# Optimization experiments

Measured on AMD Instinct MI355X. Metric: run time of the kernel, lower is better.

The kernel has to match this reference:

```python
import jax, jax.numpy as jnp
import numpy as np

NUM_CAMS, NUM_LEVELS, NUM_PTS, NUM_GROUPS = 6, 4, 13, 8


def grid_sample(fm, grid):
    """Bilinear grid_sample, align_corners=False, zeros padding.
    fm: (N,C,H,W); grid: (N,P,Q,2) xy in [-1,1] -> (N,C,P,Q)."""
    N, C, H, W = fm.shape
    x, y = grid[..., 0], grid[..., 1]
    ix = ((x + 1.0) * W - 1.0) * 0.5
    iy = ((y + 1.0) * H - 1.0) * 0.5
    ix0f = jnp.floor(ix)
    iy0f = jnp.floor(iy)
    wx1 = ix - ix0f
    wy1 = iy - iy0f
    wx0 = 1.0 - wx1
    wy0 = 1.0 - wy1
    ix0 = ix0f.astype(jnp.int32)
    iy0 = iy0f.astype(jnp.int32)
    flat = fm.reshape(N, C, H * W)

    def gather(iyc, ixc):
        valid = ((ixc >= 0) & (ixc < W) & (iyc >= 0) & (iyc < H)).astype(fm.dtype)
        idx = jnp.clip(iyc, 0, H - 1) * W + jnp.clip(ixc, 0, W - 1)
        g = jnp.take_along_axis(flat, idx.reshape(N, 1, -1), axis=2)
        return g.reshape((N, C) + idx.shape[1:]) * valid[:, None]

    v00 = gather(iy0, ix0)
    v01 = gather(iy0, ix0 + 1)
    v10 = gather(iy0 + 1, ix0)
    v11 = gather(iy0 + 1, ix0 + 1)
    return (v00 * (wy0 * wx0)[:, None] + v01 * (wy0 * wx1)[:, None]
            + v10 * (wy1 * wx0)[:, None] + v11 * (wy1 * wx1)[:, None])


def setup_inputs() -> dict:
    key = jax.random.key(0)
    ks = jax.random.split(key, 16)
    bs, NA, E = 2, 900, 256
    shapes = [(12, E, 64, 176), (12, E, 32, 88), (12, E, 16, 44), (12, E, 8, 22)]
    proj = jnp.eye(4, dtype=jnp.float32)[None, None] + 0.1 * jax.random.normal(ks[0], (bs, NUM_CAMS, 4, 4), jnp.float32)
    return {
        "instance_feature": jax.random.normal(ks[1], (bs, NA, E), jnp.float32),
        "anchor": jax.random.normal(ks[2], (bs, NA, E), jnp.float32),
        "anchor_embed": jax.random.normal(ks[3], (bs, NA, E), jnp.float32),
        "fm0": jax.random.normal(ks[4], shapes[0], jnp.float32),
        "fm1": jax.random.normal(ks[5], shapes[1], jnp.float32),
        "fm2": jax.random.normal(ks[6], shapes[2], jnp.float32),
        "fm3": jax.random.normal(ks[7], shapes[3], jnp.float32),
        "projection_mat": proj,
        "W_kps": 0.02 * jax.random.normal(ks[8], (E, NUM_PTS * 3), jnp.float32),
        "b_kps": jnp.zeros((NUM_PTS * 3,), jnp.float32),
        "W_wfc": 0.02 * jax.random.normal(ks[9], (E, NUM_GROUPS * NUM_CAMS * NUM_LEVELS * NUM_PTS), jnp.float32),
        "b_wfc": jnp.zeros((NUM_GROUPS * NUM_CAMS * NUM_LEVELS * NUM_PTS,), jnp.float32),
        "W_out": 0.02 * jax.random.normal(ks[10], (E, E), jnp.float32),
        "b_out": jnp.zeros((E,), jnp.float32),
    }


def reference(instance_feature, anchor, anchor_embed, fm0, fm1, fm2, fm3,
              projection_mat, W_kps, b_kps, W_wfc, b_wfc, W_out, b_out):
    bs, NA, E = instance_feature.shape
    C, L, P, G = NUM_CAMS, NUM_LEVELS, NUM_PTS, NUM_GROUPS
    gd = E // G
    # key points: anchor center + learned offsets (kps_generator)
    offs = (instance_feature @ W_kps + b_kps).reshape(bs, NA, P, 3)
    key_points = anchor[:, :, None, :3] + offs  # (bs,NA,P,3)
    # fusion weights: softmax over cam*level*pt slots, per group
    feat = instance_feature + anchor_embed
    w = (feat @ W_wfc + b_wfc).reshape(bs, NA, C * L * P, G)
    w = jax.nn.softmax(w, axis=-2)
    # project points to 2D
    pts = jnp.concatenate([key_points, jnp.ones_like(key_points[..., :1])], axis=-1)
    p2d = jnp.einsum('bcij,bnpj->bcnpi', projection_mat, pts)  # (bs,C,NA,P,4)
    depth = 1.0 / jnp.clip(p2d[..., 2:3], 1e-5)
    grid = (p2d[..., :2] * depth).reshape(bs * C, NA, P, 2)
    # multi-level bilinear sampling
    samples = [grid_sample(fm, grid) for fm in (fm0, fm1, fm2, fm3)]  # (bs*C,E,NA,P)
    feats = jnp.concatenate(samples, axis=3)  # (bs*C,E,NA,L*P)
    feats = feats.reshape(bs, C, E, NA, L * P).transpose(0, 3, 1, 4, 2)
    feats = feats.reshape(bs, NA, C * L * P, E)
    # grouped weighted fusion over all cam/level/pt slots
    fused = (w[..., None] * feats.reshape(bs, NA, C * L * P, G, gd)).sum(axis=2)
    fused = fused.reshape(bs, NA, E)
    out = fused @ W_out + b_out
    return out + instance_feature
```

## Files before the change

kernel.cpp:

```cpp
#include <hip/hip_runtime.h>
#include <hip/hip_bf16.h>

#define C_NUM_CAMS 6
#define C_NUM_LEVELS 4
#define C_NUM_PTS 13
#define C_NUM_GROUPS 8
#define C_BS 2
#define C_NA 900
#define C_E 256
#define C_NSLOT 312
#define C_NCOL 2496
#define C_NANCH 1800

#define LB0 0
#define LB1 34603008
#define LB2 43253760
#define LB3 45416448
#define FM8_WS_BYTES 45957120ull
#define WGT_WS_BYTES 17971200ull
#define WBT_WS_BYTES 1277952ull

typedef float floatx2 __attribute__((ext_vector_type(2)));
typedef float f32x4 __attribute__((ext_vector_type(4)));
typedef short s16x8 __attribute__((ext_vector_type(8)));
typedef float f32x4v __attribute__((ext_vector_type(4)));

static __device__ __forceinline__ int pk_fp8(float a, float b, float c, float d) {
  int v = __builtin_amdgcn_cvt_pk_fp8_f32(a, b, 0, false);
  v = __builtin_amdgcn_cvt_pk_fp8_f32(c, d, v, true);
  return v;
}
static __device__ __forceinline__ unsigned short f2bf(float f) {
  __hip_bfloat16 h = __float2bfloat16(f);
  return *reinterpret_cast<unsigned short*>(&h);
}

__global__ __launch_bounds__(256) void dfa_prep_wbt(
    const float* __restrict__ W, unsigned short* __restrict__ Wbt) {
  __shared__ unsigned short tile[64][264];
  int t = threadIdx.x;
  int c0 = blockIdx.x * 64;
  int rA = t >> 4;
  int cA = (t & 15) * 4;
#pragma unroll
  for (int p = 0; p < 16; ++p) {
    int r = p * 16 + rA;
    f32x4 v = *(const f32x4*)(W + (size_t)r * C_NCOL + c0 + cA);
    tile[cA + 0][r] = f2bf(v.x);
    tile[cA + 1][r] = f2bf(v.y);
    tile[cA + 2][r] = f2bf(v.z);
    tile[cA + 3][r] = f2bf(v.w);
  }
  __syncthreads();
  int cB = t >> 5;
  int i4 = t & 31;
#pragma unroll
  for (int p = 0; p < 8; ++p) {
    int c = p * 8 + cB;
    int4 o = *(const int4*)&tile[c][i4 * 8];
    *(int4*)(Wbt + (size_t)(c0 + c) * 256 + i4 * 8) = o;
  }
}

__global__ __launch_bounds__(256) void dfa_stage1(
    const float* __restrict__ fm0, const float* __restrict__ fm1,
    const float* __restrict__ fm2, const float* __restrict__ fm3,
    unsigned char* __restrict__ outw,
    const float* __restrict__ IF, const float* __restrict__ AE,
    const unsigned short* __restrict__ Wbt, const float* __restrict__ bwfc,
    float* __restrict__ logits) {
  __shared__ __align__(16) char smem[66560];
  int id = blockIdx.x;
  int t = threadIdx.x;
  int w = t >> 6, lane = t & 63;

  if (id >= 300) {
    int tid = id - 300;
    int (*lds)[260] = (int(*)[260])smem;
    const float* fm;
    int HW, strips;
    long long base;
    int rem;
    if (tid < 528)      { rem = tid;       fm = fm0; HW = 11264; strips = 44; base = LB0; }
    else if (tid < 660) { rem = tid - 528; fm = fm1; HW = 2816;  strips = 11; base = LB1; }
    else if (tid < 696) { rem = tid - 660; fm = fm2; HW = 704;   strips = 3;  base = LB2; }
    else                { rem = tid - 696; fm = fm3; HW = 176;   strips = 1;  base = LB3; }
    int img = rem / strips;
    int px0 = (rem % strips) * 256;

    {
      int pxl = lane * 4;
      bool pv = (px0 + pxl) < HW;
      const float* src = fm + (size_t)img * 256 * HW + px0 + pxl;
      if (pv) {
#pragma unroll 4
        for (int cq = 0; cq < 16; ++cq) {
          int ch = w * 64 + cq * 4;
          const float* s = src + (size_t)ch * HW;
          f32x4 r0 = *(const f32x4*)(s);
          f32x4 r1 = *(const f32x4*)(s + HW);
          f32x4 r2 = *(const f32x4*)(s + 2 * (size_t)HW);
          f32x4 r3 = *(const f32x4*)(s + 3 * (size_t)HW);
          int4 o;
          o.x = pk_fp8(r0.x, r1.x, r2.x, r3.x);
          o.y = pk_fp8(r0.y, r1.y, r2.y, r3.y);
          o.z = pk_fp8(r0.z, r1.z, r2.z, r3.z);
          o.w = pk_fp8(r0.w, r1.w, r2.w, r3.w);
          *(int4*)&lds[w * 16 + cq][pxl] = o;
        }
      }
    }
    __syncthreads();
    {
      int cq16 = (lane & 15) * 4;
      int pxs = lane >> 4;
#pragma unroll 4
      for (int i = 0; i < 16; ++i) {
        int px = w * 64 + i * 4 + pxs;
        if (px0 + px < HW) {
          int4 o;
          o.x = lds[cq16 + 0][px];
          o.y = lds[cq16 + 1][px];
          o.z = lds[cq16 + 2][px];
          o.w = lds[cq16 + 3][px];
          *(int4*)(outw + base + ((long long)img * HW + px0 + px) * 256 + cq16 * 4) = o;
        }
      }
    }
  } else {
    typedef unsigned short us40[40];
    us40* As = (us40*)smem;
    us40* Bs = (us40*)(smem + 10240);
    int rem = id;
    int m0 = (rem % 15) * 128;
    int n0 = (rem / 15) * 128;

    f32x4v acc[4][4];
#pragma unroll
    for (int mi = 0; mi < 4; ++mi)
#pragma unroll
      for (int ni = 0; ni < 4; ++ni)
        acc[mi][ni] = (f32x4v){0.f, 0.f, 0.f, 0.f};

    int r = t >> 1;
    int half = (t & 1) * 16;
    int wr = (w >> 1) * 64, wc = (w & 1) * 64;
    int rsel = lane & 15;
    int koff = (lane >> 4) * 8;

    for (int ks = 0; ks < 8; ++ks) {
      int k0 = ks * 32;
      {
        int a = m0 + r;
        s16x8 o0 = {0, 0, 0, 0, 0, 0, 0, 0};
        s16x8 o1 = {0, 0, 0, 0, 0, 0, 0, 0};
        if (a < C_NANCH) {
          const float* pI = IF + (size_t)a * 256 + k0 + half;
          const float* pA = AE + (size_t)a * 256 + k0 + half;
          f32x4 i0 = *(const f32x4*)(pI + 0), i1 = *(const f32x4*)(pI + 4);
          f32x4 i2 = *(const f32x4*)(pI + 8), i3 = *(const f32x4*)(pI + 12);
          f32x4 a0 = *(const f32x4*)(pA + 0), a1 = *(const f32x4*)(pA + 4);
          f32x4 a2 = *(const f32x4*)(pA + 8), a3 = *(const f32x4*)(pA + 12);
          o0[0] = (short)f2bf(i0.x + a0.x); o0[1] = (short)f2bf(i0.y + a0.y);
          o0[2] = (short)f2bf(i0.z + a0.z); o0[3] = (short)f2bf(i0.w + a0.w);
          o0[4] = (short)f2bf(i1.x + a1.x); o0[5] = (short)f2bf(i1.y + a1.y);
          o0[6] = (short)f2bf(i1.z + a1.z); o0[7] = (short)f2bf(i1.w + a1.w);
          o1[0] = (short)f2bf(i2.x + a2.x); o1[1] = (short)f2bf(i2.y + a2.y);
          o1[2] = (short)f2bf(i2.z + a2.z); o1[3] = (short)f2bf(i2.w + a2.w);
          o1[4] = (short)f2bf(i3.x + a3.x); o1[5] = (short)f2bf(i3.y + a3.y);
          o1[6] = (short)f2bf(i3.z + a3.z); o1[7] = (short)f2bf(i3.w + a3.w);
        }
        *(s16x8*)&As[r][half] = o0;
        *(s16x8*)&As[r][half + 8] = o1;
      }
      {
        int c = n0 + r;
        s16x8 b0 = {0, 0, 0, 0, 0, 0, 0, 0};
        s16x8 b1 = {0, 0, 0, 0, 0, 0, 0, 0};
        if (c < C_NCOL) {
          const unsigned short* p = Wbt + (size_t)c * 256 + k0 + half;
          b0 = *(const s16x8*)(p);
          b1 = *(const s16x8*)(p + 8);
        }
        *(s16x8*)&Bs[r][half] = b0;
        *(s16x8*)&Bs[r][half + 8] = b1;
      }
      __syncthreads();

      s16x8 af[4], bf[4];
#pragma unroll
      for (int mi = 0; mi < 4; ++mi)
        af[mi] = *(const s16x8*)&As[wr + mi * 16 + rsel][koff];
#pragma unroll
      for (int ni = 0; ni < 4; ++ni)
        bf[ni] = *(const s16x8*)&Bs[wc + ni * 16 + rsel][koff];
#pragma unroll
      for (int mi = 0; mi < 4; ++mi)
#pragma unroll
        for (int ni = 0; ni < 4; ++ni)
          acc[mi][ni] = __builtin_amdgcn_mfma_f32_16x16x32_bf16(
              af[mi], bf[ni], acc[mi][ni], 0, 0, 0);
      __syncthreads();
    }

    int rowb = (lane >> 4) * 4;
    int colo = lane & 15;
#pragma unroll
    for (int ni = 0; ni < 4; ++ni) {
      int col = n0 + wc + ni * 16 + colo;
      if (col >= C_NCOL) continue;
      float bias = bwfc[col];
#pragma unroll
      for (int mi = 0; mi < 4; ++mi) {
#pragma unroll
        for (int j = 0; j < 4; ++j) {
          int row = m0 + wr + mi * 16 + rowb + j;
          if (row < C_NANCH)
            logits[(size_t)row * C_NCOL + col] = acc[mi][ni][j] + bias;
        }
      }
    }
  }
}

__global__ __launch_bounds__(256) void dfa_agg_full(
    const unsigned char* __restrict__ fmws,
    const float* __restrict__ logits,
    const float* __restrict__ IF, const float* __restrict__ anchor,
    const float* __restrict__ Wkps, const float* __restrict__ bkps,
    const float* __restrict__ projm,
    const float* __restrict__ Wout, const float* __restrict__ bout,
    float* __restrict__ out) {
  int bn = blockIdx.x;
  int b = bn / C_NA;
  int t = threadIdx.x;
  int w = t >> 6, lane = t & 63;

  __shared__ __align__(16) float logitsS[8 * 312];
  __shared__ __align__(16) float swgt[C_NCOL];
  __shared__ unsigned short csS[1248];
  __shared__ __align__(16) float partS[8][256];
  __shared__ __align__(16) float fusedS[256];
  __shared__ float kpS[13][3];
  __shared__ float invS[8];

  int2* centry = (int2*)logitsS;
  float2* gridS = (float2*)fusedS;

  for (int i = t; i < C_NCOL; i += 256) {
    float v = logits[(size_t)bn * C_NCOL + i];
    logitsS[(i & 7) * 312 + (i >> 3)] = v;
  }
  __syncthreads();

  {
    int g = t >> 5, l32 = t & 31;
    float* row = logitsS + g * 312;
    float m = -1e30f;
    for (int s = l32; s < C_NSLOT; s += 32) m = fmaxf(m, row[s]);
#pragma unroll
    for (int off = 16; off; off >>= 1) m = fmaxf(m, __shfl_xor(m, off, 32));
    float sum = 0.f;
    for (int s = l32; s < C_NSLOT; s += 32) {
      float e = __expf(row[s] - m);
      row[s] = e;
      sum += e;
    }
#pragma unroll
    for (int off = 16; off; off >>= 1) sum += __shfl_xor(sum, off, 32);
    if (l32 == 0) invS[g] = 1.f / sum;
  }
  __syncthreads();

  for (int i = t; i < C_NCOL; i += 256)
    swgt[i] = logitsS[(i & 7) * 312 + (i >> 3)] * invS[i & 7];
  if (t < 39) {
    const float* f = IF + (size_t)bn * 256;
    float a0 = 0.f, a1 = 0.f, a2 = 0.f, a3 = 0.f;
    for (int d = 0; d < 256; d += 4) {
      a0 = fmaf(f[d + 0], Wkps[(d + 0) * 39 + t], a0);
      a1 = fmaf(f[d + 1], Wkps[(d + 1) * 39 + t], a1);
      a2 = fmaf(f[d + 2], Wkps[(d + 2) * 39 + t], a2);
      a3 = fmaf(f[d + 3], Wkps[(d + 3) * 39 + t], a3);
    }
    float acc = bkps[t] + ((a0 + a1) + (a2 + a3));
    int p = t / 3, ax = t % 3;
    kpS[p][ax] = anchor[(size_t)bn * 256 + ax] + acc;
  }
  __syncthreads();

  if (t < 78) {
    int c = t / 13, p = t % 13;
    const float* M = projm + (size_t)(b * 6 + c) * 16;
    float kx = kpS[p][0], ky = kpS[p][1], kz = kpS[p][2];
    float x = M[0] * kx + M[1] * ky + M[2] * kz + M[3];
    float y = M[4] * kx + M[5] * ky + M[6] * kz + M[7];
    float z = M[8] * kx + M[9] * ky + M[10] * kz + M[11];
    float zc = fmaxf(z, 1e-5f);
    float inv = 1.0f / zc;
    gridS[t] = make_float2(x * inv, y * inv);
  }
  __syncthreads();

  int cnt = 0;
  {
    int ebase = w * 312;
#pragma unroll
    for (int r = 0; r < 2; ++r) {
      int li = r * 64 + lane;
      bool lv = li < 78;
      int s = w * 78 + (lv ? li : 0);
      int cam = s / 52, rr = s % 52, l = rr / 13, p = rr % 13;
      float2 g2 = gridS[cam * 13 + p];
      int Wi = (l == 0) ? 176 : (l == 1) ? 88 : (l == 2) ? 44 : 22;
      int Hi = (l == 0) ? 64 : (l == 1) ? 32 : (l == 2) ? 16 : 8;
      float Wf = (float)Wi, Hf = (float)Hi;
      float ix = ((g2.x + 1.0f) * Wf - 1.0f) * 0.5f;
      float iy = ((g2.y + 1.0f) * Hf - 1.0f) * 0.5f;
      float ix0 = floorf(ix), iy0 = floorf(iy);
      float wx1 = ix - ix0, wy1 = iy - iy0;
      float wx0 = 1.f - wx1, wy0 = 1.f - wy1;
      bool vx0 = (ix0 >= 0.f) && (ix0 < Wf);
      bool vx1 = (ix0 + 1.f >= 0.f) && (ix0 + 1.f < Wf);
      bool vy0 = (iy0 >= 0.f) && (iy0 < Hf);
      bool vy1 = (iy0 + 1.f >= 0.f) && (iy0 + 1.f < Hf);
      int xi0 = (int)fminf(fmaxf(ix0, 0.f), Wf - 1.f);
      int xi1 = (int)fminf(fmaxf(ix0 + 1.f, 0.f), Wf - 1.f);
      int yi0 = (int)fminf(fmaxf(iy0, 0.f), Hf - 1.f);
      int yi1 = (int)fminf(fmaxf(iy0 + 1.f, 0.f), Hf - 1.f);
      int lb = (l == 0) ? LB0 : (l == 1) ? LB1 : (l == 2) ? LB2 : LB3;
      int ib = lb + (b * 6 + cam) * Wi * Hi * 256;
      float cw[4];
      int co[4];
      cw[0] = (vx0 && vy0) ? wy0 * wx0 : 0.f;
      cw[1] = (vx1 && vy0) ? wy0 * wx1 : 0.f;
      cw[2] = (vx0 && vy1) ? wy1 * wx0 : 0.f;
      cw[3] = (vx1 && vy1) ? wy1 * wx1 : 0.f;
      co[0] = ib + (yi0 * Wi + xi0) * 256;
      co[1] = ib + (yi0 * Wi + xi1) * 256;
      co[2] = ib + (yi1 * Wi + xi0) * 256;
      co[3] = ib + (yi1 * Wi + xi1) * 256;
      unsigned short sw8 = (unsigned short)(s * 8);
#pragma unroll
      for (int k = 0; k < 4; ++k) {
        bool v = lv && (cw[k] != 0.f);
        unsigned long long mb = __ballot(v);
        int pos = cnt + __popcll(mb & ((1ull << lane) - 1ull));
        if (v) {
          centry[ebase + pos] = make_int2(co[k], __float_as_int(cw[k]));
          csS[ebase + pos] = sw8;
        }
        cnt += (int)__popcll(mb);
      }
    }
    if (cnt & 1) {
      if (lane == 0) {
        centry[ebase + cnt] = make_int2(0, 0);
        csS[ebase + cnt] = 0;
      }
      cnt++;
    }
  }

  int half = lane >> 5, l32 = lane & 31;
  int ch = l32 * 8;
  int g = l32 >> 2;
  float acc[8];
#pragma unroll
  for (int j = 0; j < 8; ++j) acc[j] = 0.f;
  {
    int ebase = w * 312;
    int nIter = cnt >> 1;
#pragma unroll 8
    for (int i = 0; i < nIter; ++i) {
      int idx = ebase + 2 * i + half;
      int2 e = centry[idx];
      float wgt_s = swgt[(int)csS[idx] + g];
      float cw = __int_as_float(e.y) * wgt_s;
      int2 u = *reinterpret_cast<const int2*>(fmws + e.x + ch);
      floatx2 p0 = __builtin_amdgcn_cvt_pk_f32_fp8(u.x, false);
      floatx2 p1 = __builtin_amdgcn_cvt_pk_f32_fp8(u.x, true);
      floatx2 p2 = __builtin_amdgcn_cvt_pk_f32_fp8(u.y, false);
      floatx2 p3 = __builtin_amdgcn_cvt_pk_f32_fp8(u.y, true);
      acc[0] = fmaf(cw, p0.x, acc[0]);
      acc[1] = fmaf(cw, p0.y, acc[1]);
      acc[2] = fmaf(cw, p1.x, acc[2]);
      acc[3] = fmaf(cw, p1.y, acc[3]);
      acc[4] = fmaf(cw, p2.x, acc[4]);
      acc[5] = fmaf(cw, p2.y, acc[5]);
      acc[6] = fmaf(cw, p3.x, acc[6]);
      acc[7] = fmaf(cw, p3.y, acc[7]);
    }
  }
  {
    int row = w * 2 + half;
    float4 v0 = make_float4(acc[0], acc[1], acc[2], acc[3]);
    float4 v1 = make_float4(acc[4], acc[5], acc[6], acc[7]);
    *reinterpret_cast<float4*>(&partS[row][ch]) = v0;
    *reinterpret_cast<float4*>(&partS[row][ch + 4]) = v1;
  }
  __syncthreads();

  float fv = 0.f;
#pragma unroll
  for (int r = 0; r < 8; ++r) fv += partS[r][t];
  fusedS[t] = fv;
  __syncthreads();

  float o = bout[t] + IF[(size_t)bn * 256 + t];
#pragma unroll 8
  for (int d = 0; d < 256; ++d)
    o = fmaf(fusedS[d], Wout[d * 256 + t], o);
  out[(size_t)bn * 256 + t] = o;
}

__global__ __launch_bounds__(256) void dfa_logits_gemm_fb(
    const float* __restrict__ IF, const float* __restrict__ AE,
    const float* __restrict__ Wwfc, const float* __restrict__ bwfc,
    float* __restrict__ logits) {
  __shared__ float feat_t[256][16];
  int t = threadIdx.x;
  int a0 = blockIdx.x * 15;
  int col = blockIdx.y * 256 + t;
  bool cv = col < C_NCOL;
#pragma unroll
  for (int a = 0; a < 15; ++a) {
    int bn = a0 + a;
    feat_t[t][a] = IF[(size_t)bn * 256 + t] + AE[(size_t)bn * 256 + t];
  }
  feat_t[t][15] = 0.f;
  __syncthreads();
  float acc[15];
  float bias = cv ? bwfc[col] : 0.f;
#pragma unroll
  for (int a = 0; a < 15; ++a) acc[a] = bias;
  const float* wp = Wwfc + col;
#pragma unroll 8
  for (int d = 0; d < 256; ++d) {
    float wv = cv ? wp[(size_t)d * C_NCOL] : 0.f;
#pragma unroll
    for (int a = 0; a < 15; ++a) acc[a] = fmaf(feat_t[d][a], wv, acc[a]);
  }
  if (cv) {
#pragma unroll
    for (int a = 0; a < 15; ++a)
      logits[(size_t)(a0 + a) * C_NCOL + col] = acc[a];
  }
}

__global__ __launch_bounds__(256) void dfa_softmax(float* __restrict__ wgt) {
  int bn = blockIdx.x;
  float* w = wgt + (size_t)bn * C_NCOL;
  __shared__ float buf[C_NCOL];
  int t = threadIdx.x;
  for (int i = t; i < C_NCOL; i += 256) buf[i] = w[i];
  __syncthreads();
  int g = t >> 5, lane = t & 31;
  float m = -1e30f;
  for (int s = lane; s < C_NSLOT; s += 32) m = fmaxf(m, buf[s * 8 + g]);
#pragma unroll
  for (int off = 16; off; off >>= 1) m = fmaxf(m, __shfl_xor(m, off, 32));
  float sum = 0.f;
  for (int s = lane; s < C_NSLOT; s += 32) {
    float e = expf(buf[s * 8 + g] - m);
    buf[s * 8 + g] = e;
    sum += e;
  }
#pragma unroll
  for (int off = 16; off; off >>= 1) sum += __shfl_xor(sum, off, 32);
  float inv = 1.f / sum;
  for (int s = lane; s < C_NSLOT; s += 32) w[s * 8 + g] = buf[s * 8 + g] * inv;
}

__global__ __launch_bounds__(128) void dfa_points(
    const float* __restrict__ IF, const float* __restrict__ anchor,
    const float* __restrict__ Wkps, const float* __restrict__ bkps,
    const float* __restrict__ projm, float2* __restrict__ grid) {
  int bn = blockIdx.x;
  int b = bn / C_NA;
  int t = threadIdx.x;
  __shared__ float kp[13][3];
  if (t < 39) {
    float acc = bkps[t];
    const float* f = IF + (size_t)bn * 256;
    for (int d = 0; d < 256; ++d) acc = fmaf(f[d], Wkps[d * 39 + t], acc);
    int p = t / 3, ax = t % 3;
    kp[p][ax] = anchor[(size_t)bn * 256 + ax] + acc;
  }
  __syncthreads();
  if (t < 78) {
    int c = t / 13, p = t % 13;
    const float* M = projm + (size_t)(b * 6 + c) * 16;
    float kx = kp[p][0], ky = kp[p][1], kz = kp[p][2];
    float x = M[0] * kx + M[1] * ky + M[2] * kz + M[3];
    float y = M[4] * kx + M[5] * ky + M[6] * kz + M[7];
    float z = M[8] * kx + M[9] * ky + M[10] * kz + M[11];
    float zc = fmaxf(z, 1e-5f);
    float inv = 1.0f / zc;
    grid[(size_t)bn * 78 + t] = make_float2(x * inv, y * inv);
  }
}

struct __align__(16) SlotInfo { int o[4]; float w[4]; };

__global__ __launch_bounds__(256) void dfa_agg_fb(
    const float* __restrict__ fm0, const float* __restrict__ fm1,
    const float* __restrict__ fm2, const float* __restrict__ fm3,
    const float2* __restrict__ grid, const float* __restrict__ wgt,
    const float* __restrict__ IF, const float* __restrict__ Wout,
    const float* __restrict__ bout, float* __restrict__ out) {
  int bn = blockIdx.x;
  int b = bn / C_NA;
  int t = threadIdx.x;
  int w = t >> 6, lane = t & 63;

  __shared__ SlotInfo slot[C_NSLOT];
  __shared__ int sflag[C_NSLOT];
  __shared__ float swgt[C_NCOL];
  __shared__ float part[4][256];
  __shared__ float fused[256];

  for (int i = t; i < C_NCOL; i += 256) swgt[i] = wgt[(size_t)bn * C_NCOL + i];

  for (int s = t; s < C_NSLOT; s += 256) {
    int c = s / 52, r = s % 52, l = r / 13, p = r % 13;
    float2 g2 = grid[(size_t)bn * 78 + c * 13 + p];
    int Wi = (l == 0) ? 176 : (l == 1) ? 88 : (l == 2) ? 44 : 22;
    int Hi = (l == 0) ? 64 : (l == 1) ? 32 : (l == 2) ? 16 : 8;
    float Wf = (float)Wi, Hf = (float)Hi;
    float ix = ((g2.x + 1.0f) * Wf - 1.0f) * 0.5f;
    float iy = ((g2.y + 1.0f) * Hf - 1.0f) * 0.5f;
    float ix0 = floorf(ix), iy0 = floorf(iy);
    float wx1 = ix - ix0, wy1 = iy - iy0;
    float wx0 = 1.f - wx1, wy0 = 1.f - wy1;
    bool vx0 = (ix0 >= 0.f) && (ix0 < Wf);
    bool vx1 = (ix0 + 1.f >= 0.f) && (ix0 + 1.f < Wf);
    bool vy0 = (iy0 >= 0.f) && (iy0 < Hf);
    bool vy1 = (iy0 + 1.f >= 0.f) && (iy0 + 1.f < Hf);
    int xi0 = (int)fminf(fmaxf(ix0, 0.f), Wf - 1.f);
    int xi1 = (int)fminf(fmaxf(ix0 + 1.f, 0.f), Wf - 1.f);
    int yi0 = (int)fminf(fmaxf(iy0, 0.f), Hf - 1.f);
    int yi1 = (int)fminf(fmaxf(iy0 + 1.f, 0.f), Hf - 1.f);
    int img = b * 6 + c;
    int HW = Wi * Hi;
    SlotInfo si;
    int ib = img * 256 * HW;
    si.o[0] = ib + yi0 * Wi + xi0;
    si.o[1] = ib + yi0 * Wi + xi1;
    si.o[2] = ib + yi1 * Wi + xi0;
    si.o[3] = ib + yi1 * Wi + xi1;
    si.w[0] = (vx0 && vy0) ? wy0 * wx0 : 0.f;
    si.w[1] = (vx1 && vy0) ? wy0 * wx1 : 0.f;
    si.w[2] = (vx0 && vy1) ? wy1 * wx0 : 0.f;
    si.w[3] = (vx1 && vy1) ? wy1 * wx1 : 0.f;
    slot[s] = si;
    sflag[s] = (si.w[0] + si.w[1] + si.w[2] + si.w[3] == 0.f) ? -1 : l;
  }
  __syncthreads();

  int g = lane >> 3;
  int ch = lane * 4;
  float4 acc = make_float4(0.f, 0.f, 0.f, 0.f);
  for (int s = w; s < C_NSLOT; s += 4) {
    int fl = sflag[s];
    if (fl < 0) continue;
    SlotInfo si = slot[s];
    float wg = swgt[s * 8 + g];
    const float* fp = (fl == 0) ? fm0 : (fl == 1) ? fm1 : (fl == 2) ? fm2 : fm3;
    int HW = (fl == 0) ? 11264 : (fl == 1) ? 2816 : (fl == 2) ? 704 : 176;
    float4 sv = make_float4(0.f, 0.f, 0.f, 0.f);
#pragma unroll
    for (int k = 0; k < 4; ++k) {
      if (si.w[k] != 0.f) {
        sv.x = fmaf(si.w[k], fp[si.o[k] + (size_t)(ch + 0) * HW], sv.x);
        sv.y = fmaf(si.w[k], fp[si.o[k] + (size_t)(ch + 1) * HW], sv.y);
        sv.z = fmaf(si.w[k], fp[si.o[k] + (size_t)(ch + 2) * HW], sv.z);
        sv.w = fmaf(si.w[k], fp[si.o[k] + (size_t)(ch + 3) * HW], sv.w);
      }
    }
    acc.x = fmaf(sv.x, wg, acc.x);
    acc.y = fmaf(sv.y, wg, acc.y);
    acc.z = fmaf(sv.z, wg, acc.z);
    acc.w = fmaf(sv.w, wg, acc.w);
  }
  *reinterpret_cast<float4*>(&part[w][ch]) = acc;
  __syncthreads();

  fused[t] = part[0][t] + part[1][t] + part[2][t] + part[3][t];
  __syncthreads();

  float o = bout[t] + IF[(size_t)bn * 256 + t];
#pragma unroll 4
  for (int d = 0; d < 256; ++d)
    o = fmaf(fused[d], Wout[d * 256 + t], o);
  out[(size_t)bn * 256 + t] = o;
}

extern "C" void kernel_launch(void* const* d_in, const int* in_sizes, int n_in,
                              void* d_out, int out_size, void* d_ws, size_t ws_size,
                              hipStream_t stream) {
  const float* IF     = (const float*)d_in[0];
  const float* anchor = (const float*)d_in[1];
  const float* AE     = (const float*)d_in[2];
  const float* fm0    = (const float*)d_in[3];
  const float* fm1    = (const float*)d_in[4];
  const float* fm2    = (const float*)d_in[5];
  const float* fm3    = (const float*)d_in[6];
  const float* projm  = (const float*)d_in[7];
  const float* Wkps   = (const float*)d_in[8];
  const float* bkps   = (const float*)d_in[9];
  const float* Wwfc   = (const float*)d_in[10];
  const float* bwfc   = (const float*)d_in[11];
  const float* Wout   = (const float*)d_in[12];
  const float* bout   = (const float*)d_in[13];
  float* out = (float*)d_out;
  char* ws = (char*)d_ws;

  bool full = ws_size >= (FM8_WS_BYTES + WGT_WS_BYTES + WBT_WS_BYTES);
  if (full) {
    unsigned char* fmws = (unsigned char*)ws;
    float* wgt = (float*)(ws + FM8_WS_BYTES);
    unsigned short* wbt = (unsigned short*)(ws + FM8_WS_BYTES + WGT_WS_BYTES);
    dfa_prep_wbt<<<39, 256, 0, stream>>>(Wwfc, wbt);
    dfa_stage1<<<1008, 256, 0, stream>>>(fm0, fm1, fm2, fm3, fmws,
                                         IF, AE, wbt, bwfc, wgt);
    dfa_agg_full<<<1800, 256, 0, stream>>>(fmws, wgt, IF, anchor, Wkps, bkps,
                                           projm, Wout, bout, out);
  } else {
    float* wgt  = (float*)ws;
    float2* grd = (float2*)(ws + WGT_WS_BYTES);
    dfa_logits_gemm_fb<<<dim3(120, 10), 256, 0, stream>>>(IF, AE, Wwfc, bwfc, wgt);
    dfa_softmax<<<1800, 256, 0, stream>>>(wgt);
    dfa_points<<<1800, 128, 0, stream>>>(IF, anchor, Wkps, bkps, projm, grd);
    dfa_agg_fb<<<1800, 256, 0, stream>>>(fm0, fm1, fm2, fm3, grd, wgt,
                                         IF, Wout, bout, out);
  }
}
```

Before: 121.4 us.

## Split feature-map fp8 conversion into streaming pass plus byte transpose; store logits as bf16

The feature-map NCHW-to-NHWC fp8 conversion is split in two. First a fully coalesced, grid-strided fp32-to-fp8 pass runs in NCHW order alongside the logits GEMM. Then a separate kernel does the channel-last transpose on the already-shrunk fp8 bytes, using byte permutes. The aim is to replace strided fp32 reads with contiguous streaming and to make the transpose move four times fewer bytes. The logits are also written and read as bf16, halving that traffic at some precision cost. In exchange it adds a kernel launch, an extra fp8 buffer round trip and a larger workspace requirement.

```diff
diff --git a/kernel.cpp b/kernel.cpp
--- a/kernel.cpp
+++ b/kernel.cpp
@@ -17,8 +17,9 @@
 #define LB2 43253760
 #define LB3 45416448
 #define FM8_WS_BYTES 45957120ull
-#define WGT_WS_BYTES 17971200ull
+#define WGT16_WS_BYTES 8985600ull
 #define WBT_WS_BYTES 1277952ull
+#define NCH16 2872320
 
 typedef float floatx2 __attribute__((ext_vector_type(2)));
 typedef float f32x4 __attribute__((ext_vector_type(4)));
@@ -33,6 +34,12 @@
 static __device__ __forceinline__ unsigned short f2bf(float f) {
   __hip_bfloat16 h = __float2bfloat16(f);
   return *reinterpret_cast<unsigned short*>(&h);
+}
+static __device__ __forceinline__ float bf2f(unsigned short u) {
+  unsigned int v = ((unsigned int)u) << 16;
+  float f;
+  __builtin_memcpy(&f, &v, 4);
+  return f;
 }
 
 __global__ __launch_bounds__(256) void dfa_prep_wbt(
@@ -65,75 +72,44 @@
 __global__ __launch_bounds__(256) void dfa_stage1(
     const float* __restrict__ fm0, const float* __restrict__ fm1,
     const float* __restrict__ fm2, const float* __restrict__ fm3,
-    unsigned char* __restrict__ outw,
+    unsigned char* __restrict__ fm8n,
     const float* __restrict__ IF, const float* __restrict__ AE,
     const unsigned short* __restrict__ Wbt, const float* __restrict__ bwfc,
-    float* __restrict__ logits) {
-  __shared__ __align__(16) char smem[66560];
+    unsigned short* __restrict__ logits) {
+  __shared__ __align__(16) char smem[20480];
   int id = blockIdx.x;
   int t = threadIdx.x;
   int w = t >> 6, lane = t & 63;
 
   if (id >= 300) {
-    int tid = id - 300;
-    int (*lds)[260] = (int(*)[260])smem;
-    const float* fm;
-    int HW, strips;
-    long long base;
-    int rem;
-    if (tid < 528)      { rem = tid;       fm = fm0; HW = 11264; strips = 44; base = LB0; }
-    else if (tid < 660) { rem = tid - 528; fm = fm1; HW = 2816;  strips = 11; base = LB1; }
-    else if (tid < 696) { rem = tid - 660; fm = fm2; HW = 704;   strips = 3;  base = LB2; }
-    else                { rem = tid - 696; fm = fm3; HW = 176;   strips = 1;  base = LB3; }
-    int img = rem / strips;
-    int px0 = (rem % strips) * 256;
-
-    {
-      int pxl = lane * 4;
-      bool pv = (px0 + pxl) < HW;
-      const float* src = fm + (size_t)img * 256 * HW + px0 + pxl;
-      if (pv) {
-#pragma unroll 4
-        for (int cq = 0; cq < 16; ++cq) {
-          int ch = w * 64 + cq * 4;
-          const float* s = src + (size_t)ch * HW;
-          f32x4 r0 = *(const f32x4*)(s);
-          f32x4 r1 = *(const f32x4*)(s + HW);
-          f32x4 r2 = *(const f32x4*)(s + 2 * (size_t)HW);
-          f32x4 r3 = *(const f32x4*)(s + 3 * (size_t)HW);
-          int4 o;
-          o.x = pk_fp8(r0.x, r1.x, r2.x, r3.x);
-          o.y = pk_fp8(r0.y, r1.y, r2.y, r3.y);
-          o.z = pk_fp8(r0.z, r1.z, r2.z, r3.z);
-          o.w = pk_fp8(r0.w, r1.w, r2.w, r3.w);
-          *(int4*)&lds[w * 16 + cq][pxl] = o;
-        }
-      }
-    }
-    __syncthreads();
-    {
-      int cq16 = (lane & 15) * 4;
-      int pxs = lane >> 4;
-#pragma unroll 4
-      for (int i = 0; i < 16; ++i) {
-        int px = w * 64 + i * 4 + pxs;
-        if (px0 + px < HW) {
-          int4 o;
-          o.x = lds[cq16 + 0][px];
-          o.y = lds[cq16 + 1][px];
-          o.z = lds[cq16 + 2][px];
-          o.w = lds[cq16 + 3][px];
-          *(int4*)(outw + base + ((long long)img * HW + px0 + px) * 256 + cq16 * 4) = o;
-        }
-      }
+    int pid = id - 300;
+    for (long long c16 = (long long)pid * 256 + t; c16 < NCH16;
+         c16 += 1748ll * 256) {
+      long long eb = c16 * 16;
+      const float* src;
+      long long off;
+      if (eb < LB1)      { src = fm0; off = eb - LB0; }
+      else if (eb < LB2) { src = fm1; off = eb - LB1; }
+      else if (eb < LB3) { src = fm2; off = eb - LB2; }
+      else               { src = fm3; off = eb - LB3; }
+      const float* p = src + off;
+      f32x4 a0 = *(const f32x4*)(p + 0);
+      f32x4 a1 = *(const f32x4*)(p + 4);
+      f32x4 a2 = *(const f32x4*)(p + 8);
+      f32x4 a3 = *(const f32x4*)(p + 12);
+      int4 o;
+      o.x = pk_fp8(a0.x, a0.y, a0.z, a0.w);
+      o.y = pk_fp8(a1.x, a1.y, a1.z, a1.w);
+      o.z = pk_fp8(a2.x, a2.y, a2.z, a2.w);
+      o.w = pk_fp8(a3.x, a3.y, a3.z, a3.w);
+      *(int4*)(fm8n + eb) = o;
     }
   } else {
     typedef unsigned short us40[40];
     us40* As = (us40*)smem;
     us40* Bs = (us40*)(smem + 10240);
-    int rem = id;
-    int m0 = (rem % 15) * 128;
-    int n0 = (rem / 15) * 128;
+    int m0 = (id % 15) * 128;
+    int n0 = (id / 15) * 128;
 
     f32x4v acc[4][4];
 #pragma unroll
@@ -216,8 +192,78 @@
         for (int j = 0; j < 4; ++j) {
           int row = m0 + wr + mi * 16 + rowb + j;
           if (row < C_NANCH)
-            logits[(size_t)row * C_NCOL + col] = acc[mi][ni][j] + bias;
+            logits[(size_t)row * C_NCOL + col] = f2bf(acc[mi][ni][j] + bias);
         }
+      }
+    }
+  }
+}
+
+__global__ __launch_bounds__(256) void dfa_tr2(
+    const unsigned char* __restrict__ fm8n, unsigned char* __restrict__ out) {
+  int id = blockIdx.x;
+  int HW, strips;
+  long long base;
+  int rem;
+  if (id < 528)      { rem = id;       HW = 11264; strips = 44; base = LB0; }
+  else if (id < 660) { rem = id - 528; HW = 2816;  strips = 11; base = LB1; }
+  else if (id < 696) { rem = id - 660; HW = 704;   strips = 3;  base = LB2; }
+  else               { rem = id - 696; HW = 176;   strips = 1;  base = LB3; }
+  int img = rem / strips;
+  int px0 = (rem % strips) * 256;
+
+  __shared__ int lds[64][260];
+  int t = threadIdx.x;
+  int w = t >> 6, lane = t & 63;
+
+  {
+    int pxl = lane * 4;
+    bool pv = (px0 + pxl) < HW;
+    const unsigned char* srcb = fm8n + base + (size_t)img * 256 * HW + px0 + pxl;
+    if (pv) {
+#pragma unroll 4
+      for (int cq = 0; cq < 16; ++cq) {
+        int c = w * 64 + cq * 4;
+        const unsigned char* s = srcb + (size_t)c * HW;
+        unsigned r0 = *(const unsigned*)(s);
+        unsigned r1 = *(const unsigned*)(s + HW);
+        unsigned r2 = *(const unsigned*)(s + 2 * (size_t)HW);
+        unsigned r3 = *(const unsigned*)(s + 3 * (size_t)HW);
+        int4 o;
+        {
+          unsigned tA, tB;
+          tA = __builtin_amdgcn_perm(r1, r0, 0x00000400u);
+          tB = __builtin_amdgcn_perm(r3, r2, 0x00000400u);
+          o.x = (int)__builtin_amdgcn_perm(tB, tA, 0x05040100u);
+          tA = __builtin_amdgcn_perm(r1, r0, 0x00000501u);
+          tB = __builtin_amdgcn_perm(r3, r2, 0x00000501u);
+          o.y = (int)__builtin_amdgcn_perm(tB, tA, 0x05040100u);
+          tA = __builtin_amdgcn_perm(r1, r0, 0x00000602u);
+          tB = __builtin_amdgcn_perm(r3, r2, 0x00000602u);
+          o.z = (int)__builtin_amdgcn_perm(tB, tA, 0x05040100u);
+          tA = __builtin_amdgcn_perm(r1, r0, 0x00000703u);
+          tB = __builtin_amdgcn_perm(r3, r2, 0x00000703u);
+          o.w = (int)__builtin_amdgcn_perm(tB, tA, 0x05040100u);
+        }
+        *(int4*)&lds[w * 16 + cq][pxl] = o;
+      }
+    }
+  }
+  __syncthreads();
+
+  {
+    int cq16 = (lane & 15) * 4;
+    int pxs = lane >> 4;
+#pragma unroll 4
+    for (int i = 0; i < 16; ++i) {
+      int px = w * 64 + i * 4 + pxs;
+      if (px0 + px < HW) {
+        int4 o;
+        o.x = lds[cq16 + 0][px];
+        o.y = lds[cq16 + 1][px];
+        o.z = lds[cq16 + 2][px];
+        o.w = lds[cq16 + 3][px];
+        *(int4*)(out + base + ((long long)img * HW + px0 + px) * 256 + cq16 * 4) = o;
       }
     }
   }
@@ -225,7 +271,7 @@
 
 __global__ __launch_bounds__(256) void dfa_agg_full(
     const unsigned char* __restrict__ fmws,
-    const float* __restrict__ logits,
+    const unsigned short* __restrict__ logits,
     const float* __restrict__ IF, const float* __restrict__ anchor,
     const float* __restrict__ Wkps, const float* __restrict__ bkps,
     const float* __restrict__ projm,
@@ -248,7 +294,7 @@
   float2* gridS = (float2*)fusedS;
 
   for (int i = t; i < C_NCOL; i += 256) {
-    float v = logits[(size_t)bn * C_NCOL + i];
+    float v = bf2f(logits[(size_t)bn * C_NCOL + i]);
     logitsS[(i & 7) * 312 + (i >> 3)] = v;
   }
   __syncthreads();
@@ -616,19 +662,21 @@
   float* out = (float*)d_out;
   char* ws = (char*)d_ws;
 
-  bool full = ws_size >= (FM8_WS_BYTES + WGT_WS_BYTES + WBT_WS_BYTES);
+  bool full = ws_size >= (2 * FM8_WS_BYTES + WGT16_WS_BYTES + WBT_WS_BYTES);
   if (full) {
     unsigned char* fmws = (unsigned char*)ws;
-    float* wgt = (float*)(ws + FM8_WS_BYTES);
-    unsigned short* wbt = (unsigned short*)(ws + FM8_WS_BYTES + WGT_WS_BYTES);
+    unsigned char* fm8n = (unsigned char*)(ws + FM8_WS_BYTES);
+    unsigned short* wgt16 = (unsigned short*)(ws + 2 * FM8_WS_BYTES);
+    unsigned short* wbt = (unsigned short*)(ws + 2 * FM8_WS_BYTES + WGT16_WS_BYTES);
     dfa_prep_wbt<<<39, 256, 0, stream>>>(Wwfc, wbt);
-    dfa_stage1<<<1008, 256, 0, stream>>>(fm0, fm1, fm2, fm3, fmws,
-                                         IF, AE, wbt, bwfc, wgt);
-    dfa_agg_full<<<1800, 256, 0, stream>>>(fmws, wgt, IF, anchor, Wkps, bkps,
+    dfa_stage1<<<2048, 256, 0, stream>>>(fm0, fm1, fm2, fm3, fm8n,
+                                         IF, AE, wbt, bwfc, wgt16);
+    dfa_tr2<<<708, 256, 0, stream>>>(fm8n, fmws);
+    dfa_agg_full<<<1800, 256, 0, stream>>>(fmws, wgt16, IF, anchor, Wkps, bkps,
                                            projm, Wout, bout, out);
   } else {
     float* wgt  = (float*)ws;
-    float2* grd = (float2*)(ws + WGT_WS_BYTES);
+    float2* grd = (float2*)(ws + 17971200ull);
     dfa_logits_gemm_fb<<<dim3(120, 10), 256, 0, stream>>>(IF, AE, Wwfc, bwfc, wgt);
     dfa_softmax<<<1800, 256, 0, stream>>>(wgt);
     dfa_points<<<1800, 128, 0, stream>>>(IF, anchor, Wkps, bkps, projm, grd);
```

Measured after the change: 139.4 us. 1.15x slower.
